# Optimization experiments

Hardware: AMD Instinct MI355X
Metric: run time of the kernel (lower is better)

## Reference

```python
import jax, jax.numpy as jnp
import numpy as np

EPS = 1e-12  # matches torch F.normalize eps

def _l2norm(x, axis):
    n = jnp.sqrt(jnp.sum(x * x, axis=axis, keepdims=True))
    return x / jnp.maximum(n, EPS)

def setup_inputs() -> dict:
    key = jax.random.key(0)
    k1, k2, k3, k4 = jax.random.split(key, 4)
    b, n_way, k_shot, q, c, h, w = 2, 5, 5, 75, 64, 21, 21
    return {
        "support_xf": jax.random.normal(k1, (b, n_way * k_shot, c, h, w), dtype=jnp.float32),
        "support_y": jax.random.randint(k2, (b, n_way * k_shot), 0, n_way),
        "query_xf": jax.random.normal(k3, (b, q, c, h, w), dtype=jnp.float32),
        "query_y": jax.random.randint(k4, (b, q), 0, n_way),
        "n_way": n_way,
        "k_shot": k_shot,
    }

def reference(support_xf, support_y, query_xf, query_y, n_way, k_shot):
    b, q, c, h, w = query_xf.shape
    hw = h * w
    # k_shot averaging: (b, n_way, k_shot, c, h, w) -> mean over shots -> (b, n_way, c, hw)
    sup = support_xf.reshape(b, n_way, k_shot, c, hw).mean(axis=2)
    qry = query_xf.reshape(b, q, c, hw)
    # cosine similarity: L2-normalize each local descriptor along channel dim
    sup_n = _l2norm(sup, axis=2)  # (b, n_way, c, hw_s)
    qry_n = _l2norm(qry, axis=2)  # (b, q, c, hw_q)
    # inner product matrix: (b, q, n_way, hw_q, hw_s)
    sim = jnp.einsum('bqcm,bwcn->bqwmn', qry_n, sup_n)
    # topk with k=1 along support descriptors, mean over k == max
    topv = jnp.max(sim, axis=-1)  # (b, q, n_way, hw_q)
    logits = topv.sum(axis=-1).reshape(b * q, n_way)  # image-to-class score
    return logits
```

## Files before the change

### kernel.cpp

```cpp
#include <hip/hip_runtime.h>
#include <hip/hip_bf16.h>

namespace {
constexpr int kB = 2, kW = 5, kS = 5, kQ = 75, kC = 64, kHW = 441;
constexpr int kNP = 448;
constexpr int kMP = 448;
constexpr int kCHUNK = 112;
constexpr int kLDT = 65;
constexpr int kSupUnits = kB * kW * 4;
constexpr int kUnits = kSupUnits + kB * kQ * 4;
constexpr int kTiles = kB * kQ * kW;
constexpr int kThreads = 448;
constexpr int kWaves = 7;

typedef short bf16x8 __attribute__((ext_vector_type(8)));
typedef float f32x16 __attribute__((ext_vector_type(16)));
typedef __attribute__((address_space(3))) unsigned int lds_u32;
typedef const __attribute__((address_space(1))) unsigned int gbl_u32;
}

__global__ __launch_bounds__(256) void prep_k(const float* __restrict__ sup,
                                              const float* __restrict__ qry,
                                              unsigned short* __restrict__ snT,
                                              unsigned short* __restrict__ qnT) {
  __shared__ float img_t[kCHUNK * kLDT];
  __shared__ float inv[kCHUNK];
  const int tid = threadIdx.x;
  const int blk = blockIdx.x;

  int m0, mcnt;
  unsigned short* dst;
  const bool is_sup = blk < kSupUnits;

  if (is_sup) {
    int bw = blk >> 2, chunk = blk & 3;
    m0 = chunk * kCHUNK;
    mcnt = min(kCHUNK, kHW - m0);
    const float* base = sup + (size_t)bw * kS * kC * kHW;
    for (int i = tid; i < kC * kCHUNK; i += 256) {
      int c = i / kCHUNK, mm = i % kCHUNK;
      float v = 0.f;
      if (mm < mcnt) {
        const float* p = base + (size_t)c * kHW + m0 + mm;
        float s = 0.f;
#pragma unroll
        for (int k = 0; k < kS; ++k) s += p[(size_t)k * kC * kHW];
        v = s * (1.f / kS);
      }
      img_t[mm * kLDT + c] = v;
    }
    dst = snT + (size_t)bw * kNP * kC;
  } else {
    int qb = blk - kSupUnits;
    int bq = qb >> 2, chunk = qb & 3;
    m0 = chunk * kCHUNK;
    mcnt = min(kCHUNK, kHW - m0);
    const float* base = qry + (size_t)bq * kC * kHW;
    for (int i = tid; i < kC * kCHUNK; i += 256) {
      int c = i / kCHUNK, mm = i % kCHUNK;
      img_t[mm * kLDT + c] = (mm < mcnt) ? base[(size_t)c * kHW + m0 + mm] : 0.f;
    }
    dst = qnT + (size_t)bq * kMP * kC;
  }
  __syncthreads();

  if (tid < kCHUNK) {
    float ss = 0.f;
#pragma unroll
    for (int c = 0; c < kC; ++c) { float v = img_t[tid * kLDT + c]; ss += v * v; }
    inv[tid] = 1.f / fmaxf(sqrtf(ss), 1e-12f);
  }
  __syncthreads();

  for (int i8 = tid; i8 < kCHUNK * 8; i8 += 256) {
    int m = i8 >> 3, c8 = (i8 & 7) * 8;
    float sc = inv[m];
    union { unsigned short u[8]; uint4 v; } pk;
#pragma unroll
    for (int j = 0; j < 8; ++j) {
      __hip_bfloat16 o = __float2bfloat16(img_t[m * kLDT + c8 + j] * sc);
      pk.u[j] = *reinterpret_cast<unsigned short*>(&o);
    }
    *reinterpret_cast<uint4*>(dst + ((size_t)(m0 + m) * kC + c8)) = pk.v;
  }
}

__device__ __forceinline__ float max16_v(const f32x16& a) {
  float m0 = fmaxf(fmaxf(a[0], a[1]), a[2]);
  float m1 = fmaxf(fmaxf(a[3], a[4]), a[5]);
  float m2 = fmaxf(fmaxf(a[6], a[7]), a[8]);
  float m3 = fmaxf(fmaxf(a[9], a[10]), a[11]);
  float m4 = fmaxf(fmaxf(a[12], a[13]), a[14]);
  return fmaxf(fmaxf(fmaxf(m0, m1), m2), fmaxf(fmaxf(m3, m4), a[15]));
}
__device__ __forceinline__ float max12_v(const f32x16& a) {
  float m0 = fmaxf(fmaxf(a[0], a[1]), a[2]);
  float m1 = fmaxf(fmaxf(a[3], a[4]), a[5]);
  float m2 = fmaxf(fmaxf(a[6], a[7]), a[8]);
  float m3 = fmaxf(fmaxf(a[9], a[10]), a[11]);
  return fmaxf(fmaxf(m0, m1), fmaxf(m2, m3));
}

template <bool TAIL_HALF>
__device__ __forceinline__ void compute_half(const unsigned short* As,
                                             const bf16x8 bf[2][4],
                                             int lane, float rm[2]) {
  const int lh = lane >> 5;
  const int lm = lane & 31;
  f32x16 z;
#pragma unroll
  for (int r = 0; r < 16; ++r) z[r] = 0.f;

#pragma unroll 1
  for (int ntl = 0; ntl < 7; ++ntl) {
    bf16x8 af[4];
    int n = ntl * 32 + lm;
#pragma unroll
    for (int kk = 0; kk < 4; ++kk) {
      int k16 = kk * 2 + lh;
      af[kk] = *reinterpret_cast<const bf16x8*>(As + ((size_t)(n * 8 + (k16 ^ (n & 7))) << 3));
    }
    if (!TAIL_HALF || ntl < 6) {
#pragma unroll
      for (int ct = 0; ct < 2; ++ct) {
        f32x16 acc = z;
#pragma unroll
        for (int kk = 0; kk < 4; ++kk)
          acc = __builtin_amdgcn_mfma_f32_32x32x16_bf16(af[kk], bf[ct][kk], acc, 0, 0, 0);
        rm[ct] = fmaxf(rm[ct], max16_v(acc));
      }
    } else {
#pragma unroll
      for (int ct = 0; ct < 2; ++ct) {
        f32x16 acc = z;
#pragma unroll
        for (int kk = 0; kk < 4; ++kk)
          acc = __builtin_amdgcn_mfma_f32_32x32x16_bf16(af[kk], bf[ct][kk], acc, 0, 0, 0);
        float t = max12_v(acc);
        if (lh == 0) t = fmaxf(t, acc[12]);
        rm[ct] = fmaxf(rm[ct], t);
      }
    }
  }
}

__global__ __launch_bounds__(kThreads) void dn4_main_k(const unsigned short* __restrict__ qnT,
                                                       const unsigned short* __restrict__ snT,
                                                       float* __restrict__ out) {
  __shared__ __align__(16) unsigned short As[224 * kC];
  __shared__ float part[kWaves];
  const int tid = threadIdx.x;

  const int xcd = blockIdx.x & 7, jj = blockIdx.x >> 3;
  const int idx = (xcd < 6) ? xcd * 94 + jj : 564 + (xcd - 6) * 93 + jj;

  const int w = idx % kW;
  const int bq = idx / kW;
  const int b = bq / kQ;

  const int lane = tid & 63;
  const int lh = lane >> 5;
  const int lm = lane & 31;
  const int wid = tid >> 6;
  const int ct0 = wid * 2;

  const char* sbase = (const char*)(snT + (size_t)(b * kW + w) * kNP * kC);
  const unsigned short* qb = qnT + (size_t)bq * kMP * kC;

#pragma unroll
  for (int it = 0; it < 4; ++it) {
    int L = it * kThreads + tid;
    int srcj = (L & ~7) | ((L & 7) ^ ((L >> 3) & 7));
    __builtin_amdgcn_global_load_lds((gbl_u32*)(sbase + ((size_t)srcj << 4)),
                                     (lds_u32*)((char*)As + ((size_t)L << 4)), 16, 0, 0);
  }

  bf16x8 bf[2][4];
#pragma unroll
  for (int ct = 0; ct < 2; ++ct) {
    int m = (ct0 + ct) * 32 + lm;
#pragma unroll
    for (int kk = 0; kk < 4; ++kk)
      bf[ct][kk] = *reinterpret_cast<const bf16x8*>(qb + (size_t)m * kC + kk * 16 + lh * 8);
  }

  float rm[2] = {-INFINITY, -INFINITY};

  __syncthreads();
  compute_half<false>(As, bf, lane, rm);
  __syncthreads();

#pragma unroll
  for (int it = 0; it < 4; ++it) {
    int L = it * kThreads + tid;
    int srcj = (L & ~7) | ((L & 7) ^ ((L >> 3) & 7));
    __builtin_amdgcn_global_load_lds((gbl_u32*)(sbase + ((size_t)(1792 + srcj) << 4)),
                                     (lds_u32*)((char*)As + ((size_t)L << 4)), 16, 0, 0);
  }
  __syncthreads();
  compute_half<true>(As, bf, lane, rm);

  float s = fmaxf(rm[0], __shfl_xor(rm[0], 32, 64)) +
            fmaxf(rm[1], __shfl_xor(rm[1], 32, 64));
#pragma unroll
  for (int off = 1; off < 32; off <<= 1) s += __shfl_xor(s, off, 64);

  if (lane == 0) part[wid] = s;
  __syncthreads();
  if (tid == 0) {
    float t = 0.f;
#pragma unroll
    for (int v = 0; v < kWaves; ++v) t += part[v];
    out[idx] = t;
  }
}

extern "C" void kernel_launch(void* const* d_in, const int* in_sizes, int n_in,
                              void* d_out, int out_size, void* d_ws, size_t ws_size,
                              hipStream_t stream) {
  const float* sup = (const float*)d_in[0];
  const float* qry = (const float*)d_in[2];
  float* out = (float*)d_out;

  unsigned short* snT = (unsigned short*)d_ws;
  unsigned short* qnT = snT + (size_t)kB * kW * kNP * kC;

  prep_k<<<kUnits, 256, 0, stream>>>(sup, qry, snT, qnT);
  dn4_main_k<<<kTiles, kThreads, 0, stream>>>(qnT, snT, out);
}
```

Baseline: 39.11 us.

## Read support tiles directly from global memory instead of staging through LDS

The main kernel no longer copies the normalized support descriptors into shared memory with global_load_lds in two halves separated by barriers. Each wave now loads its A fragments straight from global memory (through L1/L2) in a single 14-tile loop. This removes the LDS staging, the swizzle and three block barriers, and frees LDS for higher occupancy. In exchange, all 7 waves read the same support data redundantly from cache, and global-load latency is exposed inside the MFMA loop.

```diff
diff --git a/kernel.cpp b/kernel.cpp
--- a/kernel.cpp
+++ b/kernel.cpp
@@ -15,8 +15,6 @@
 
 typedef short bf16x8 __attribute__((ext_vector_type(8)));
 typedef float f32x16 __attribute__((ext_vector_type(16)));
-typedef __attribute__((address_space(3))) unsigned int lds_u32;
-typedef const __attribute__((address_space(1))) unsigned int gbl_u32;
 }
 
 __global__ __launch_bounds__(256) void prep_k(const float* __restrict__ sup,
@@ -101,53 +99,9 @@
   return fmaxf(fmaxf(m0, m1), fmaxf(m2, m3));
 }
 
-template <bool TAIL_HALF>
-__device__ __forceinline__ void compute_half(const unsigned short* As,
-                                             const bf16x8 bf[2][4],
-                                             int lane, float rm[2]) {
-  const int lh = lane >> 5;
-  const int lm = lane & 31;
-  f32x16 z;
-#pragma unroll
-  for (int r = 0; r < 16; ++r) z[r] = 0.f;
-
-#pragma unroll 1
-  for (int ntl = 0; ntl < 7; ++ntl) {
-    bf16x8 af[4];
-    int n = ntl * 32 + lm;
-#pragma unroll
-    for (int kk = 0; kk < 4; ++kk) {
-      int k16 = kk * 2 + lh;
-      af[kk] = *reinterpret_cast<const bf16x8*>(As + ((size_t)(n * 8 + (k16 ^ (n & 7))) << 3));
-    }
-    if (!TAIL_HALF || ntl < 6) {
-#pragma unroll
-      for (int ct = 0; ct < 2; ++ct) {
-        f32x16 acc = z;
-#pragma unroll
-        for (int kk = 0; kk < 4; ++kk)
-          acc = __builtin_amdgcn_mfma_f32_32x32x16_bf16(af[kk], bf[ct][kk], acc, 0, 0, 0);
-        rm[ct] = fmaxf(rm[ct], max16_v(acc));
-      }
-    } else {
-#pragma unroll
-      for (int ct = 0; ct < 2; ++ct) {
-        f32x16 acc = z;
-#pragma unroll
-        for (int kk = 0; kk < 4; ++kk)
-          acc = __builtin_amdgcn_mfma_f32_32x32x16_bf16(af[kk], bf[ct][kk], acc, 0, 0, 0);
-        float t = max12_v(acc);
-        if (lh == 0) t = fmaxf(t, acc[12]);
-        rm[ct] = fmaxf(rm[ct], t);
-      }
-    }
-  }
-}
-
 __global__ __launch_bounds__(kThreads) void dn4_main_k(const unsigned short* __restrict__ qnT,
                                                        const unsigned short* __restrict__ snT,
                                                        float* __restrict__ out) {
-  __shared__ __align__(16) unsigned short As[224 * kC];
   __shared__ float part[kWaves];
   const int tid = threadIdx.x;
 
@@ -164,16 +118,8 @@
   const int wid = tid >> 6;
   const int ct0 = wid * 2;
 
-  const char* sbase = (const char*)(snT + (size_t)(b * kW + w) * kNP * kC);
+  const unsigned short* sb = snT + (size_t)(b * kW + w) * kNP * kC;
   const unsigned short* qb = qnT + (size_t)bq * kMP * kC;
-
-#pragma unroll
-  for (int it = 0; it < 4; ++it) {
-    int L = it * kThreads + tid;
-    int srcj = (L & ~7) | ((L & 7) ^ ((L >> 3) & 7));
-    __builtin_amdgcn_global_load_lds((gbl_u32*)(sbase + ((size_t)srcj << 4)),
-                                     (lds_u32*)((char*)As + ((size_t)L << 4)), 16, 0, 0);
-  }
 
   bf16x8 bf[2][4];
 #pragma unroll
@@ -184,21 +130,46 @@
       bf[ct][kk] = *reinterpret_cast<const bf16x8*>(qb + (size_t)m * kC + kk * 16 + lh * 8);
   }
 
+  f32x16 z;
+#pragma unroll
+  for (int r = 0; r < 16; ++r) z[r] = 0.f;
   float rm[2] = {-INFINITY, -INFINITY};
 
-  __syncthreads();
-  compute_half<false>(As, bf, lane, rm);
-  __syncthreads();
-
-#pragma unroll
-  for (int it = 0; it < 4; ++it) {
-    int L = it * kThreads + tid;
-    int srcj = (L & ~7) | ((L & 7) ^ ((L >> 3) & 7));
-    __builtin_amdgcn_global_load_lds((gbl_u32*)(sbase + ((size_t)(1792 + srcj) << 4)),
-                                     (lds_u32*)((char*)As + ((size_t)L << 4)), 16, 0, 0);
-  }
-  __syncthreads();
-  compute_half<true>(As, bf, lane, rm);
+  const unsigned short* arow = sb + (size_t)lm * kC + lh * 8;
+
+#pragma unroll 1
+  for (int nt = 0; nt < 13; ++nt) {
+    bf16x8 af[4];
+    const unsigned short* p = arow + (size_t)nt * 32 * kC;
+#pragma unroll
+    for (int kk = 0; kk < 4; ++kk)
+      af[kk] = *reinterpret_cast<const bf16x8*>(p + kk * 16);
+#pragma unroll
+    for (int ct = 0; ct < 2; ++ct) {
+      f32x16 acc = z;
+#pragma unroll
+      for (int kk = 0; kk < 4; ++kk)
+        acc = __builtin_amdgcn_mfma_f32_32x32x16_bf16(af[kk], bf[ct][kk], acc, 0, 0, 0);
+      rm[ct] = fmaxf(rm[ct], max16_v(acc));
+    }
+  }
+  {
+    bf16x8 af[4];
+    const unsigned short* p = arow + (size_t)13 * 32 * kC;
+#pragma unroll
+    for (int kk = 0; kk < 4; ++kk)
+      af[kk] = *reinterpret_cast<const bf16x8*>(p + kk * 16);
+#pragma unroll
+    for (int ct = 0; ct < 2; ++ct) {
+      f32x16 acc = z;
+#pragma unroll
+      for (int kk = 0; kk < 4; ++kk)
+        acc = __builtin_amdgcn_mfma_f32_32x32x16_bf16(af[kk], bf[ct][kk], acc, 0, 0, 0);
+      float t = max12_v(acc);
+      if (lh == 0) t = fmaxf(t, acc[12]);
+      rm[ct] = fmaxf(rm[ct], t);
+    }
+  }
 
   float s = fmaxf(rm[0], __shfl_xor(rm[0], 32, 64)) +
             fmaxf(rm[1], __shfl_xor(rm[1], 32, 64));
```

Result: slower. 60.84 us (+55.6%).
